# Performance work log

Measured on AMD Instinct MI355X. Metric: run time of the kernel, lower is better.

The kernel has to match this reference:

```python
import jax, jax.numpy as jnp
import numpy as np

N_NODES = 100000
N_EDGES = 1600000
D_IN = 64
D_OUT = 64
K_HOPS = 2


def setup_inputs() -> dict:
    key = jax.random.key(0)
    k1, k2, k3, k4 = jax.random.split(key, 4)
    x = jax.random.normal(k1, (N_NODES, D_IN), dtype=jnp.float32)
    W = jax.random.normal(k2, (D_OUT, D_IN), dtype=jnp.float32) * (1.0 / np.sqrt(D_IN))
    b = jax.random.normal(k3, (D_OUT,), dtype=jnp.float32) * 0.01
    edge_index = jax.random.randint(k4, (2, N_EDGES), 0, N_NODES, dtype=jnp.int64)
    return {"x": x, "W": W, "b": b, "edge_index": edge_index}


def reference(x, W, b, edge_index):
    # SGConv (K=2) with gcn_norm + self-loops, then Linear, then ReLU.
    # Dropout is identity in eval mode.
    n = x.shape[0]
    self_loops = jnp.arange(n, dtype=edge_index.dtype)
    row = jnp.concatenate([edge_index[0], self_loops])  # source j
    col = jnp.concatenate([edge_index[1], self_loops])  # target i
    ones = jnp.ones(row.shape[0], dtype=x.dtype)
    deg = jax.ops.segment_sum(ones, col, num_segments=n)
    deg_inv_sqrt = jnp.where(deg > 0, jax.lax.rsqrt(deg), 0.0).astype(x.dtype)
    norm = deg_inv_sqrt[row] * deg_inv_sqrt[col]  # [E+N]
    h = x
    for _ in range(K_HOPS):
        h = jax.ops.segment_sum(norm[:, None] * h[row], col, num_segments=n)
    out = h @ W.T + b
    return jax.nn.relu(out)
```

## Files before the change

kernel.cpp:

```cpp
#include <hip/hip_runtime.h>
#include <hip/hip_fp16.h>

#define D 64
#define CAP 48
#define NBMAX 1024
#define BCAP 5120


__global__ __launch_bounds__(256) void partition_k(const int* __restrict__ row,
                                                   const int* __restrict__ col,
                                                   unsigned int* __restrict__ bcur,
                                                   unsigned int* __restrict__ part,
                                                   int E, int NB) {
    __shared__ unsigned int lcnt[NBMAX];
    __shared__ unsigned int lpos[NBMAX];
    __shared__ unsigned int lbase[NBMAX];
    int tid = threadIdx.x;
    for (int k = tid; k < NB; k += 256) { lcnt[k] = 0u; lpos[k] = 0u; }
    __syncthreads();
    int chunk = (E + (int)gridDim.x - 1) / (int)gridDim.x;
    int s = blockIdx.x * chunk, eend = min(E, s + chunk);
    for (int e = s + tid; e < eend; e += 256) atomicAdd(&lcnt[(unsigned)col[e] >> 8], 1u);
    __syncthreads();
    for (int k = tid; k < NB; k += 256) lbase[k] = lcnt[k] ? atomicAdd(&bcur[k], lcnt[k]) : 0u;
    __syncthreads();
    for (int e = s + tid; e < eend; e += 256) {
        int i = col[e];
        int bk = (unsigned)i >> 8;
        unsigned int r = lbase[bk] + atomicAdd(&lpos[bk], 1u);
        if (r < BCAP)
            part[(size_t)bk * BCAP + r] = ((unsigned int)(i & 255) << 24) | (unsigned int)row[e];
    }
}


__global__ __launch_bounds__(256) void build_k(const unsigned int* __restrict__ part,
                                               const unsigned int* __restrict__ bcur,
                                               int* __restrict__ csrp,
                                               unsigned int* __restrict__ deg,
                                               float* __restrict__ dinv,
                                               unsigned int* __restrict__ hist,
                                               const float* __restrict__ x,
                                               __half* __restrict__ xh, int n) {
    __shared__ unsigned int ldeg[256];
    __shared__ unsigned int lh[64];
    int b = blockIdx.x, tid = threadIdx.x;
    ldeg[tid] = 0u;
    if (tid < 64) lh[tid] = 0u;
    __syncthreads();
    unsigned int cnt = bcur[b]; if (cnt > BCAP) cnt = BCAP;
    int nodeBase = b << 8;
    for (unsigned int t = tid; t < cnt; t += 256) {
        unsigned int e = part[(size_t)b * BCAP + t];
        unsigned int il = e >> 24;
        unsigned int r = atomicAdd(&ldeg[il], 1u);
        if (r < CAP) csrp[(size_t)(nodeBase + il) * CAP + r] = (int)(e & 0xFFFFFFu);
    }
    __syncthreads();
    int i = nodeBase + tid;
    if (i < n) {
        unsigned int c = ldeg[tid];
        deg[i] = c;
        dinv[i] = rsqrtf((float)(c + 1u));
        atomicAdd(&lh[c < 63u ? c : 63u], 1u);
    }
    __syncthreads();
    if (tid < 64 && lh[tid]) atomicAdd(&hist[tid], lh[tid]);
    for (int t = tid; t < 256 * 16; t += 256) {
        int rl = t >> 4;
        int i2 = nodeBase + rl;
        if (i2 >= n) break;
        float s = rsqrtf((float)(ldeg[rl] + 1u));
        float4 v = ((const float4*)x)[(size_t)i2 * 16 + (t & 15)];
        union { __half2 h[2]; float2 f; } u;
        u.h[0] = __float22half2_rn(make_float2(v.x * s, v.y * s));
        u.h[1] = __float22half2_rn(make_float2(v.z * s, v.w * s));
        ((float2*)xh)[(size_t)i2 * 16 + (t & 15)] = u.f;
    }
}


__global__ void scan_k(const unsigned int* __restrict__ hist, unsigned int* __restrict__ hoff) {
    int lane = threadIdx.x & 63;
    unsigned int v = hist[lane];
    unsigned int s = v;
#pragma unroll
    for (int off = 1; off < 64; off <<= 1) {
        unsigned int t = (unsigned int)__shfl_up((int)s, off, 64);
        if (lane >= off) s += t;
    }
    hoff[lane] = s - v;
}


__global__ void order_k(const unsigned int* __restrict__ deg, unsigned int* __restrict__ hoff,
                        unsigned int* __restrict__ order, int n) {
    __shared__ unsigned int lh[64];
    __shared__ unsigned int lbase[64];
    int tid = threadIdx.x;
    if (tid < 64) lh[tid] = 0u;
    __syncthreads();
    int i = blockIdx.x * blockDim.x + tid;
    unsigned int key = 0u, lrank = 0u;
    if (i < n) {
        unsigned int c = deg[i];
        key = c < 63u ? c : 63u;
        lrank = atomicAdd(&lh[key], 1u);
    }
    __syncthreads();
    if (tid < 64) lbase[tid] = lh[tid] ? atomicAdd(&hoff[tid], lh[tid]) : 0u;
    __syncthreads();
    if (i < n) order[(unsigned int)(n - 1) - (lbase[key] + lrank)] = (unsigned int)i;
}


__device__ __forceinline__ void add_row8(float acc[8], float4 raw) {
    const __half2* q = (const __half2*)&raw;
#pragma unroll
    for (int k = 0; k < 4; ++k) {
        float2 f = __half22float2(q[k]);
        acc[2 * k]     += f.x;
        acc[2 * k + 1] += f.y;
    }
}

__device__ __forceinline__ void aggregate_node(const __half* __restrict__ h_in,
                                               const int* __restrict__ csr,
                                               uint2 sg, int fb, float acc[8]) {
    float a1[8];
#pragma unroll
    for (int k = 0; k < 8; ++k) { acc[k] = 0.0f; a1[k] = 0.0f; }
    unsigned int e = sg.x, end = sg.x + sg.y;
    for (; e + 8 <= end; e += 8) {
        int p[8];
#pragma unroll
        for (int k = 0; k < 8; ++k) p[k] = csr[e + k];
        float4 r[8];
#pragma unroll
        for (int k = 0; k < 8; ++k) r[k] = *(const float4*)(h_in + (size_t)p[k] * D + fb);
#pragma unroll
        for (int k = 0; k < 8; ++k) add_row8((k & 1) ? a1 : acc, r[k]);
    }
    if (e + 4 <= end) {
        int p0 = csr[e], p1 = csr[e + 1], p2 = csr[e + 2], p3 = csr[e + 3];
        float4 r0 = *(const float4*)(h_in + (size_t)p0 * D + fb);
        float4 r1 = *(const float4*)(h_in + (size_t)p1 * D + fb);
        float4 r2 = *(const float4*)(h_in + (size_t)p2 * D + fb);
        float4 r3 = *(const float4*)(h_in + (size_t)p3 * D + fb);
        add_row8(acc, r0);
        add_row8(a1,  r1);
        add_row8(acc, r2);
        add_row8(a1,  r3);
        e += 4;
    }
    for (; e < end; ++e) {
        int p = csr[e];
        float4 r = *(const float4*)(h_in + (size_t)p * D + fb);
        add_row8(acc, r);
    }
#pragma unroll
    for (int k = 0; k < 8; ++k) acc[k] += a1[k];
}

__device__ __forceinline__ void aggregate_node16(const __half* __restrict__ h_in,
                                                 const int* __restrict__ csr,
                                                 uint2 sg, int fb, float acc[8]) {
    float a1[8];
#pragma unroll
    for (int k = 0; k < 8; ++k) { acc[k] = 0.0f; a1[k] = 0.0f; }
    unsigned int e = sg.x, end = sg.x + sg.y;
    for (; e + 16 <= end; e += 16) {
        int p[16];
#pragma unroll
        for (int k = 0; k < 16; ++k) p[k] = csr[e + k];
        float4 r[16];
#pragma unroll
        for (int k = 0; k < 16; ++k) r[k] = *(const float4*)(h_in + (size_t)p[k] * D + fb);
#pragma unroll
        for (int k = 0; k < 16; ++k) add_row8((k & 1) ? a1 : acc, r[k]);
    }
    if (e + 8 <= end) {
        int p[8];
#pragma unroll
        for (int k = 0; k < 8; ++k) p[k] = csr[e + k];
        float4 r[8];
#pragma unroll
        for (int k = 0; k < 8; ++k) r[k] = *(const float4*)(h_in + (size_t)p[k] * D + fb);
#pragma unroll
        for (int k = 0; k < 8; ++k) add_row8((k & 1) ? a1 : acc, r[k]);
        e += 8;
    }
    if (e + 4 <= end) {
        int p0 = csr[e], p1 = csr[e + 1], p2 = csr[e + 2], p3 = csr[e + 3];
        float4 r0 = *(const float4*)(h_in + (size_t)p0 * D + fb);
        float4 r1 = *(const float4*)(h_in + (size_t)p1 * D + fb);
        float4 r2 = *(const float4*)(h_in + (size_t)p2 * D + fb);
        float4 r3 = *(const float4*)(h_in + (size_t)p3 * D + fb);
        add_row8(acc, r0);
        add_row8(a1,  r1);
        add_row8(acc, r2);
        add_row8(a1,  r3);
        e += 4;
    }
    for (; e < end; ++e) {
        int p = csr[e];
        float4 r = *(const float4*)(h_in + (size_t)p * D + fb);
        add_row8(acc, r);
    }
#pragma unroll
    for (int k = 0; k < 8; ++k) acc[k] += a1[k];
}


__global__ __launch_bounds__(256) void hop8s_k(const __half* __restrict__ h_in,
                                               const float* __restrict__ dinv,
                                               const unsigned int* __restrict__ deg,
                                               const int* __restrict__ csr,
                                               const unsigned int* __restrict__ order,
                                               __half* __restrict__ h_out, int n) {
    int wave = blockIdx.x * 4 + (threadIdx.x >> 6);
    int lane = threadIdx.x & 63;
    int g = lane >> 3;
    int fb = (lane & 7) << 3;
    int idx = wave * 8 + g;
    bool valid = (idx < n);
    int i = valid ? (int)order[idx] : 0;
    unsigned int dg = valid ? deg[i] : 0u;
    uint2 sg = make_uint2((unsigned int)i * CAP, dg < CAP ? dg : (unsigned int)CAP);
    float acc[8];
    aggregate_node16(h_in, csr, sg, fb, acc);
    if (valid) {
        float di = dinv[i];
        float s1 = di * di;
        float4 s = *(const float4*)(h_in + (size_t)i * D + fb);
        add_row8(acc, s);
        float4 outv;
        __half2* o = (__half2*)&outv;
        o[0] = __float22half2_rn(make_float2(acc[0] * s1, acc[1] * s1));
        o[1] = __float22half2_rn(make_float2(acc[2] * s1, acc[3] * s1));
        o[2] = __float22half2_rn(make_float2(acc[4] * s1, acc[5] * s1));
        o[3] = __float22half2_rn(make_float2(acc[6] * s1, acc[7] * s1));
        *(float4*)(h_out + (size_t)i * D + fb) = outv;
    }
}


__global__ __launch_bounds__(256) void hop8s_linear_k(const __half* __restrict__ h_in,
                                                      const float* __restrict__ dinv,
                                                      const unsigned int* __restrict__ deg,
                                                      const int* __restrict__ csr,
                                                      const unsigned int* __restrict__ order,
                                                      const float* __restrict__ W,
                                                      const float* __restrict__ b,
                                                      float* __restrict__ out, int n) {
    __shared__ float Wt[D][D + 1];
    __shared__ float sh[4][8][D];
    int tid = threadIdx.x;
    for (int k = tid; k < D * D; k += 256) Wt[k & 63][k >> 6] = W[k];
    __syncthreads();
    int w = tid >> 6, lane = tid & 63;
    int wave = blockIdx.x * 4 + w;
    int g = lane >> 3;
    int fb = (lane & 7) << 3;
    int idx = wave * 8 + g;
    bool valid = (idx < n);
    int i = valid ? (int)order[idx] : 0;
    unsigned int dg = valid ? deg[i] : 0u;
    uint2 sg = make_uint2((unsigned int)i * CAP, dg < CAP ? dg : (unsigned int)CAP);
    float acc[8];
    aggregate_node(h_in, csr, sg, fb, acc);
    if (valid) {
        float di = dinv[i];
        float4 s = *(const float4*)(h_in + (size_t)i * D + fb);
        add_row8(acc, s);
        *(float4*)&sh[w][g][fb]     = make_float4(acc[0] * di, acc[1] * di,
                                                  acc[2] * di, acc[3] * di);
        *(float4*)&sh[w][g][fb + 4] = make_float4(acc[4] * di, acc[5] * di,
                                                  acc[6] * di, acc[7] * di);
    }
    float bias = b[lane];
    float o[8];
#pragma unroll
    for (int nd = 0; nd < 8; ++nd) o[nd] = bias;
#pragma unroll 1
    for (int dc = 0; dc < D; dc += 8) {
        float wr[8];
#pragma unroll
        for (int k = 0; k < 8; ++k) wr[k] = Wt[dc + k][lane];
#pragma unroll
        for (int nd = 0; nd < 8; ++nd) {
            float4 s0 = *(const float4*)&sh[w][nd][dc];
            float4 s1 = *(const float4*)&sh[w][nd][dc + 4];
            o[nd] = fmaf(s0.x, wr[0], o[nd]);
            o[nd] = fmaf(s0.y, wr[1], o[nd]);
            o[nd] = fmaf(s0.z, wr[2], o[nd]);
            o[nd] = fmaf(s0.w, wr[3], o[nd]);
            o[nd] = fmaf(s1.x, wr[4], o[nd]);
            o[nd] = fmaf(s1.y, wr[5], o[nd]);
            o[nd] = fmaf(s1.z, wr[6], o[nd]);
            o[nd] = fmaf(s1.w, wr[7], o[nd]);
        }
    }
#pragma unroll 1
    for (int nd = 0; nd < 8; ++nd) {
        int idx2 = wave * 8 + nd;
        if (idx2 < n) {
            int ni = (int)order[idx2];
            __builtin_nontemporal_store(fmaxf(o[nd], 0.0f), &out[(size_t)ni * D + lane]);
        }
    }
}


extern "C" void kernel_launch(void* const* d_in, const int* in_sizes, int n_in,
                              void* d_out, int out_size, void* d_ws, size_t ws_size,
                              hipStream_t stream) {
    const float* x = (const float*)d_in[0];
    const float* W = (const float*)d_in[1];
    const float* b = (const float*)d_in[2];
    const int*   ei = (const int*)d_in[3];

    const int n = in_sizes[0] / D;
    const int E = in_sizes[3] / 2;
    const int* row = ei;
    const int* col = ei + E;
    float* out = (float*)d_out;

    char* ws = (char*)d_ws;
    size_t off = 0;
    unsigned int* deg   = (unsigned int*)(ws + off); off += (size_t)n * 4;
    float*        dinv  = (float*)(ws + off);        off += (size_t)n * 4;
    unsigned int* order = (unsigned int*)(ws + off); off += (size_t)n * 4;
    unsigned int* bcur  = (unsigned int*)(ws + off); off += (size_t)NBMAX * 4;
    unsigned int* hist  = (unsigned int*)(ws + off); off += 256;
    unsigned int* hoff  = (unsigned int*)(ws + off); off += 256;
    int*          csrp  = (int*)(ws + off);          off += (size_t)n * CAP * 4;
    __half*       xh    = (__half*)(ws + off);       off += (size_t)n * D * 2;
    __half*       h1h   = (__half*)(ws + off);       off += (size_t)n * D * 2;
    unsigned int* part  = (unsigned int*)h1h;

    const int NB = (n + 255) >> 8;
    const int nb = (n + 255) / 256;
    const int gb = (n + 31) / 32;

    hipMemsetAsync(bcur, 0, (size_t)NBMAX * 4 + 256, stream);
    partition_k<<<512, 256, 0, stream>>>(row, col, bcur, part, E, NB);
    build_k<<<NB, 256, 0, stream>>>(part, bcur, csrp, deg, dinv, hist, x, xh, n);
    scan_k<<<1, 64, 0, stream>>>(hist, hoff);
    order_k<<<nb, 256, 0, stream>>>(deg, hoff, order, n);

    hop8s_k<<<gb, 256, 0, stream>>>(xh, dinv, deg, csrp, order, h1h, n);
    hop8s_linear_k<<<gb, 256, 0, stream>>>(h1h, dinv, deg, csrp, order, W, b, out, n);
}
```

Baseline: 221.6 us.

## Split first hop into two feature-half passes with 4 lanes per node

The first propagation hop is split into two launches, each covering half of the 64 feature columns. Within each launch, 4 lanes handle one node, so a wave covers 16 nodes. The aim is to shrink the gathered working set per pass (32 half-precision columns per row) for better cache hit rates on random neighbor gathers, and to raise the number of nodes in flight. In exchange, the CSR index list is read twice and an extra kernel launch is added. The 16-way unrolled aggregate is also replaced by the simpler aggregate_node.

```diff
diff --git a/kernel.cpp b/kernel.cpp
--- a/kernel.cpp
+++ b/kernel.cpp
@@ -162,73 +162,24 @@
     for (int k = 0; k < 8; ++k) acc[k] += a1[k];
 }
 
-__device__ __forceinline__ void aggregate_node16(const __half* __restrict__ h_in,
-                                                 const int* __restrict__ csr,
-                                                 uint2 sg, int fb, float acc[8]) {
-    float a1[8];
-#pragma unroll
-    for (int k = 0; k < 8; ++k) { acc[k] = 0.0f; a1[k] = 0.0f; }
-    unsigned int e = sg.x, end = sg.x + sg.y;
-    for (; e + 16 <= end; e += 16) {
-        int p[16];
-#pragma unroll
-        for (int k = 0; k < 16; ++k) p[k] = csr[e + k];
-        float4 r[16];
-#pragma unroll
-        for (int k = 0; k < 16; ++k) r[k] = *(const float4*)(h_in + (size_t)p[k] * D + fb);
-#pragma unroll
-        for (int k = 0; k < 16; ++k) add_row8((k & 1) ? a1 : acc, r[k]);
-    }
-    if (e + 8 <= end) {
-        int p[8];
-#pragma unroll
-        for (int k = 0; k < 8; ++k) p[k] = csr[e + k];
-        float4 r[8];
-#pragma unroll
-        for (int k = 0; k < 8; ++k) r[k] = *(const float4*)(h_in + (size_t)p[k] * D + fb);
-#pragma unroll
-        for (int k = 0; k < 8; ++k) add_row8((k & 1) ? a1 : acc, r[k]);
-        e += 8;
-    }
-    if (e + 4 <= end) {
-        int p0 = csr[e], p1 = csr[e + 1], p2 = csr[e + 2], p3 = csr[e + 3];
-        float4 r0 = *(const float4*)(h_in + (size_t)p0 * D + fb);
-        float4 r1 = *(const float4*)(h_in + (size_t)p1 * D + fb);
-        float4 r2 = *(const float4*)(h_in + (size_t)p2 * D + fb);
-        float4 r3 = *(const float4*)(h_in + (size_t)p3 * D + fb);
-        add_row8(acc, r0);
-        add_row8(a1,  r1);
-        add_row8(acc, r2);
-        add_row8(a1,  r3);
-        e += 4;
-    }
-    for (; e < end; ++e) {
-        int p = csr[e];
-        float4 r = *(const float4*)(h_in + (size_t)p * D + fb);
-        add_row8(acc, r);
-    }
-#pragma unroll
-    for (int k = 0; k < 8; ++k) acc[k] += a1[k];
-}
-
-
-__global__ __launch_bounds__(256) void hop8s_k(const __half* __restrict__ h_in,
+
+__global__ __launch_bounds__(256) void hop4s_k(const __half* __restrict__ h_in,
                                                const float* __restrict__ dinv,
                                                const unsigned int* __restrict__ deg,
                                                const int* __restrict__ csr,
                                                const unsigned int* __restrict__ order,
-                                               __half* __restrict__ h_out, int n) {
+                                               __half* __restrict__ h_out, int n, int hh) {
     int wave = blockIdx.x * 4 + (threadIdx.x >> 6);
     int lane = threadIdx.x & 63;
-    int g = lane >> 3;
-    int fb = (lane & 7) << 3;
-    int idx = wave * 8 + g;
+    int g = lane >> 2;
+    int fb = ((lane & 3) << 3) + (hh << 5);
+    int idx = wave * 16 + g;
     bool valid = (idx < n);
     int i = valid ? (int)order[idx] : 0;
     unsigned int dg = valid ? deg[i] : 0u;
     uint2 sg = make_uint2((unsigned int)i * CAP, dg < CAP ? dg : (unsigned int)CAP);
     float acc[8];
-    aggregate_node16(h_in, csr, sg, fb, acc);
+    aggregate_node(h_in, csr, sg, fb, acc);
     if (valid) {
         float di = dinv[i];
         float s1 = di * di;
@@ -341,7 +292,8 @@
 
     const int NB = (n + 255) >> 8;
     const int nb = (n + 255) / 256;
-    const int gb = (n + 31) / 32;
+    const int gb  = (n + 31) / 32;
+    const int gb2 = (n + 63) / 64;
 
     hipMemsetAsync(bcur, 0, (size_t)NBMAX * 4 + 256, stream);
     partition_k<<<512, 256, 0, stream>>>(row, col, bcur, part, E, NB);
@@ -349,6 +301,7 @@
     scan_k<<<1, 64, 0, stream>>>(hist, hoff);
     order_k<<<nb, 256, 0, stream>>>(deg, hoff, order, n);
 
-    hop8s_k<<<gb, 256, 0, stream>>>(xh, dinv, deg, csrp, order, h1h, n);
+    hop4s_k<<<gb2, 256, 0, stream>>>(xh, dinv, deg, csrp, order, h1h, n, 0);
+    hop4s_k<<<gb2, 256, 0, stream>>>(xh, dinv, deg, csrp, order, h1h, n, 1);
     hop8s_linear_k<<<gb, 256, 0, stream>>>(h1h, dinv, deg, csrp, order, W, b, out, n);
 }
```

Result: slower. 255.5 us (+15.3%).
